# Optimization experiments

Hardware: AMD Instinct MI355X
Metric: run time of the kernel (lower is better)

The kernel has to match this reference:

```python
import jax, jax.numpy as jnp
import numpy as np

NUM_LEVELS = 4
RADIUS = 4


def _avg_pool2(x):
    # x: [N, H, W] -> 2x2 avg pool, stride 2, VALID (matches F.avg_pool2d(corr, 2, 2))
    s = jax.lax.reduce_window(x, 0.0, jax.lax.add, (1, 2, 2), (1, 2, 2), 'VALID')
    return s * 0.25


def _bilinear_sampler(img, coords):
    # img: [N, H, W]; coords: [N, K, K, 2] with (x, y) in pixel units.
    # Matches grid_sample(align_corners=True, padding_mode='zeros').
    N, H, W = img.shape
    x, y = coords[..., 0], coords[..., 1]
    x0 = jnp.floor(x)
    y0 = jnp.floor(y)
    nidx = jnp.arange(N)[:, None, None]

    def corner(xi, yi, w):
        valid = (xi >= 0) & (xi <= W - 1) & (yi >= 0) & (yi <= H - 1)
        xc = jnp.clip(xi, 0, W - 1).astype(jnp.int32)
        yc = jnp.clip(yi, 0, H - 1).astype(jnp.int32)
        return jnp.where(valid, img[nidx, yc, xc], 0.0) * w

    wx1 = x - x0
    wx0 = 1.0 - wx1
    wy1 = y - y0
    wy0 = 1.0 - wy1
    return (corner(x0, y0, wx0 * wy0) + corner(x0 + 1.0, y0, wx1 * wy0)
            + corner(x0, y0 + 1.0, wx0 * wy1) + corner(x0 + 1.0, y0 + 1.0, wx1 * wy1))


def setup_inputs() -> dict:
    key = jax.random.key(0)
    ks = jax.random.split(key, 8)
    B, C, H, W, D = 2, 256, 46, 96, 256
    fmap1 = jax.random.normal(ks[0], (B, C, H, W), jnp.float32)
    fmap2 = jax.random.normal(ks[1], (B, C, H, W), jnp.float32)
    ys, xs = jnp.meshgrid(jnp.arange(H, dtype=jnp.float32),
                          jnp.arange(W, dtype=jnp.float32), indexing='ij')
    base = jnp.broadcast_to(jnp.stack([xs, ys], 0), (B, 2, H, W))  # channels = (x, y)
    coords1 = base
    coords_lookup = base + 2.0 * jax.random.normal(ks[2], (B, 2, H, W), jnp.float32)
    Wf = jax.random.normal(ks[3], (C, D), jnp.float32) / np.sqrt(C).astype(np.float32)
    bf = jnp.zeros((D,), jnp.float32)
    Wpos = jax.random.normal(ks[4], (2, D), jnp.float32) * 0.003
    Wq = jax.random.normal(ks[5], (D, D), jnp.float32) / np.sqrt(D).astype(np.float32)
    Wk = jax.random.normal(ks[6], (D, D), jnp.float32) / np.sqrt(D).astype(np.float32)
    return {"fmap1": fmap1, "fmap2": fmap2, "coords1": coords1,
            "coords_lookup": coords_lookup, "Wf": Wf, "bf": bf,
            "Wpos": Wpos, "Wq": Wq, "Wk": Wk}


def reference(fmap1, fmap2, coords1, coords_lookup, Wf, bf, Wpos, Wq, Wk):
    B, C, H, W = fmap1.shape
    HW = H * W
    D = Wf.shape[1]
    dt = fmap1.dtype
    # --- update(): SETrans cross-attention correlation volume ---
    # coords2 = gen_all_indices -> full (y, x) grid
    ys, xs = jnp.meshgrid(jnp.arange(H, dtype=dt), jnp.arange(W, dtype=dt), indexing='ij')
    coords2_yx = jnp.broadcast_to(jnp.stack([ys, xs], -1), (B, H, W, 2)).reshape(B, HW, 2)
    # coords1 stored as (x, y) channels; permute(0,2,3,1).flip(-1) -> (y, x)
    coords1_yx = jnp.transpose(coords1, (0, 2, 3, 1))[..., ::-1].reshape(B, HW, 2)
    f1 = jnp.transpose(fmap1.reshape(B, C, HW), (0, 2, 1))  # [B, HW, C]
    f2 = jnp.transpose(fmap2.reshape(B, C, HW), (0, 2, 1))
    pos1 = coords1_yx @ Wpos                                  # [B, HW, D]
    pos2 = coords2_yx @ Wpos
    vispos1 = f1 @ Wf + bf + pos1
    vispos2 = f2 @ Wf + bf + pos2
    scale = jnp.sqrt(jnp.asarray(D, dt))
    pos_biases = jnp.einsum('bid,bjd->bij', pos1, pos2) / scale  # injected positional biases
    q = vispos1 @ Wq
    k = vispos2 @ Wk
    scores = jnp.einsum('bid,bjd->bij', q, k) / scale + pos_biases
    corr = jax.nn.softmax(scores, axis=-1)                    # [B, HW1, HW2] attn-prob correlation
    corr = corr.reshape(B * HW, H, W)
    pyramid = [corr]
    for _ in range(NUM_LEVELS - 1):
        corr = _avg_pool2(corr)
        pyramid.append(corr)
    # --- __call__(coords): multiscale bilinear lookup ---
    r = RADIUS
    d = jnp.linspace(-r, r, 2 * r + 1, dtype=dt)
    dyy, dxx = jnp.meshgrid(d, d, indexing='ij')              # matches torch.meshgrid(dy, dx)
    delta = jnp.stack([dyy, dxx], -1)[None]                   # [1, K, K, 2]
    cl = jnp.transpose(coords_lookup, (0, 2, 3, 1)).reshape(B * HW, 1, 1, 2)
    outs = []
    for i, lvl in enumerate(pyramid):
        coords_lvl = cl / (2.0 ** i) + delta                  # [B*HW, K, K, 2]
        samp = _bilinear_sampler(lvl, coords_lvl)             # [B*HW, K, K]
        outs.append(samp.reshape(B, H, W, -1))
    out = jnp.concatenate(outs, axis=-1)                      # [B, H, W, L*K*K]
    return jnp.transpose(out, (0, 3, 1, 2)).astype(jnp.float32)
```

## Files before the change

kernel.cpp:

```cpp
#include <hip/hip_runtime.h>
#include <cstdint>

typedef _Float16 f16;
typedef __attribute__((ext_vector_type(2))) _Float16 f16x2;
typedef __attribute__((ext_vector_type(4))) _Float16 f16x4;
typedef __attribute__((ext_vector_type(8))) _Float16 f16x8;
typedef __attribute__((ext_vector_type(4))) float f32x4;

#define NB 2
#define NH 46
#define NW 96
#define NHW 4416
#define ND 256
#define NTILES 276
#define SSTR 4424
#define L2E 1.44269504f

#define OFF_WFQ 0
#define OFF_WFK 131072
#define OFF_PQ  262144
#define OFF_PK  264192
#define OFF_BQ  266240
#define OFF_BK  267264
#define OFF_GS  268288
#define OFF_Q   268544
#define OFF_K   4790528
#define OFF_RM  9312512
#define OFF_S   9453824
#define SCOL    4432
#define WS_NEED 87740672UL

__global__ __launch_bounds__(256) void prep_kernel(
    const float* __restrict__ Wf, const float* __restrict__ bf,
    const float* __restrict__ Wpos, const float* __restrict__ Wq,
    const float* __restrict__ Wk, char* __restrict__ ws) {
  f16* WFQ = (f16*)(ws + OFF_WFQ);
  f16* WFK = (f16*)(ws + OFF_WFK);
  float* PQ = (float*)(ws + OFF_PQ);
  float* PK = (float*)(ws + OFF_PK);
  float* BQ = (float*)(ws + OFF_BQ);
  float* BK = (float*)(ws + OFF_BK);
  float* GS = (float*)(ws + OFF_GS);
  int bid = blockIdx.x, d = threadIdx.x;
  if (bid < 256) {
    int c = bid;
    float aq = 0.f, ak = 0.f;
#pragma unroll 8
    for (int t = 0; t < 256; ++t) {
      float wf = Wf[c * 256 + t];
      aq += wf * Wq[t * 256 + d];
      ak += wf * Wk[t * 256 + d];
    }
    WFQ[c * 256 + d] = (f16)(aq * 0.0625f);
    WFK[c * 256 + d] = (f16)ak;
  } else if (bid == 256) {
    float pq0 = 0, pq1 = 0, pk0 = 0, pk1 = 0, bq = 0, bk = 0;
#pragma unroll 4
    for (int c = 0; c < 256; ++c) {
      float wq = Wq[c * 256 + d], wk = Wk[c * 256 + d];
      pq0 += Wpos[c] * wq;       pq1 += Wpos[256 + c] * wq;
      pk0 += Wpos[c] * wk;       pk1 += Wpos[256 + c] * wk;
      bq  += bf[c] * wq;         bk  += bf[c] * wk;
    }
    PQ[d] = pq0 * 0.0625f; PQ[256 + d] = pq1 * 0.0625f;
    PK[d] = pk0;           PK[256 + d] = pk1;
    BQ[d] = bq * 0.0625f;  BK[d] = bk;
  } else if (d < 4) {
    int a = d >> 1, b2 = d & 1;
    float g = 0;
    for (int t = 0; t < 256; ++t) g += Wpos[a * 256 + t] * Wpos[b2 * 256 + t];
    GS[d] = g * 0.0625f;
  }
}

__global__ __launch_bounds__(256) void qk_gemm(
    const float* __restrict__ fmap1, const float* __restrict__ fmap2,
    const float* __restrict__ coords1, char* __restrict__ ws) {
  __shared__ f16 As[64 * 40];
  __shared__ f16 Bs[128 * 40];
  __shared__ float py[64], px[64];
  const int z = blockIdx.z;
  const float* fmap = z ? fmap2 : fmap1;
  const f16* Wt = (const f16*)(ws + (z ? OFF_WFK : OFF_WFQ));
  const float* P = (const float*)(ws + (z ? OFF_PK : OFF_PQ));
  const float* bias = (const float*)(ws + (z ? OFF_BK : OFF_BQ));
  f16* outb = (f16*)(ws + (z ? OFF_K : OFF_Q));
  const int t = threadIdx.x;
  const int g0 = blockIdx.x * 64;
  const int b = g0 / NHW;
  const int hwb = g0 - b * NHW;
  const int d0 = blockIdx.y * 128;
  if (t < 64) {
    int hw = hwb + t;
    if (z == 0) {
      py[t] = coords1[(b * 2 + 1) * NHW + hw];
      px[t] = coords1[(b * 2 + 0) * NHW + hw];
    } else {
      int y = hw / NW;
      py[t] = (float)y;
      px[t] = (float)(hw - y * NW);
    }
  }
  const int lane = t & 63, wave = t >> 6;
  const int wr = (wave >> 1) * 32, wc0 = (wave & 1) * 64;
  const int hwl = t & 63, cl0 = t >> 6;
  const int dd = t & 127, ch = t >> 7;
  f32x4 acc[2][4] = {};
  for (int kt = 0; kt < 8; ++kt) {
    int kk = kt * 32;
    __syncthreads();
#pragma unroll
    for (int i = 0; i < 8; ++i) {
      int c = cl0 + i * 4;
      As[hwl * 40 + c] = (f16)fmap[(size_t)(b * ND + kk + c) * NHW + hwb + hwl];
    }
#pragma unroll
    for (int i = 0; i < 16; ++i) {
      int c = ch * 16 + i;
      Bs[dd * 40 + c] = Wt[(kk + c) * ND + d0 + dd];
    }
    __syncthreads();
    int row = lane & 15, kq = (lane >> 4) * 8;
    f16x8 a0 = *(const f16x8*)&As[(wr + row) * 40 + kq];
    f16x8 a1 = *(const f16x8*)&As[(wr + 16 + row) * 40 + kq];
#pragma unroll
    for (int s = 0; s < 4; ++s) {
      f16x8 bs = *(const f16x8*)&Bs[(wc0 + 16 * s + row) * 40 + kq];
      acc[0][s] = __builtin_amdgcn_mfma_f32_16x16x32_f16(a0, bs, acc[0][s], 0, 0, 0);
      acc[1][s] = __builtin_amdgcn_mfma_f32_16x16x32_f16(a1, bs, acc[1][s], 0, 0, 0);
    }
  }
#pragma unroll
  for (int fi = 0; fi < 2; ++fi)
#pragma unroll
    for (int s = 0; s < 4; ++s)
#pragma unroll
      for (int r = 0; r < 4; ++r) {
        int rowl = wr + fi * 16 + (lane >> 4) * 4 + r;
        int d = d0 + wc0 + s * 16 + (lane & 15);
        float v = acc[fi][s][r] + bias[d] + py[rowl] * P[d] + px[rowl] * P[ND + d];
        outb[(size_t)(g0 + rowl) * ND + d] = (f16)v;
      }
}

__global__ __launch_bounds__(384, 2) void score_gemm(
    const float* __restrict__ coords1, char* __restrict__ ws) {
  __shared__ f16 kls[2][32][264];
  __shared__ f16 stw[6][16][36];
  __shared__ float u0s[96], u1s[96];
  const int tid = threadIdx.x;
  const int blk = blockIdx.x;
  const int xcd = blk & 7;
  const int b = xcd >> 2, nq = xcd & 3;
  const int hw0 = (blk >> 3) * 96;
  const int j00 = nq * 1104;
  const float* GS = (const float*)(ws + OFF_GS);
  if (tid < 96) {
    int hw = hw0 + tid;
    float cy = coords1[(b * 2 + 1) * NHW + hw];
    float cx = coords1[(b * 2 + 0) * NHW + hw];
    u0s[tid] = cy * GS[0] + cx * GS[2];
    u1s[tid] = cy * GS[1] + cx * GS[3];
  }
  const f16* __restrict__ qb = (const f16*)(ws + OFF_Q);
  const f16* __restrict__ kb = (const f16*)(ws + OFF_K);
  f16* __restrict__ gSb = (f16*)(ws + OFF_S) + ((size_t)b * NHW + hw0) * SCOL;
  float* __restrict__ rmG = (float*)(ws + OFF_RM);
  const int lane = tid & 63, wave = tid >> 6;
  const int q = lane & 15, h = lane >> 4;
  f16x8 qfrag[8];
#pragma unroll
  for (int ks = 0; ks < 8; ++ks)
    qfrag[ks] = *(const f16x8*)&qb[(size_t)(b * NHW + hw0 + wave * 16 + q) * ND + ks * 32 + h * 8];
  for (int c = tid; c < 32 * 32; c += 384) {
    int r = c >> 5, cc = c & 31;
    *(f16x8*)&kls[0][r][cc * 8] =
        *(const f16x8*)&kb[(size_t)(b * NHW + j00 + r) * ND + cc * 8];
  }
  __syncthreads();
  const float u0m = u0s[wave * 16 + q], u1m = u1s[wave * 16 + q];
  float pmax = -3e38f;
  const int srow = lane >> 2, scg = lane & 3;

  for (int it = 0; it <= 34; ++it) {
    const int buf = it & 1;
    const int jp = j00 + it * 32;
    const bool full = (it < 34);
    if (it < 34) {
      const int nW = (it < 33) ? 32 : 16;
      const int jn = j00 + (it + 1) * 32;
      for (int c = tid; c < nW * 32; c += 384) {
        int r = c >> 5, cc = c & 31;
        *(f16x8*)&kls[buf ^ 1][r][cc * 8] =
            *(const f16x8*)&kb[(size_t)(b * NHW + jn + r) * ND + cc * 8];
      }
    }
    f32x4 acc0 = {}, acc1 = {};
#pragma unroll
    for (int ks = 0; ks < 8; ++ks) {
      f16x8 kf = *(const f16x8*)&kls[buf][q][ks * 32 + h * 8];
      acc0 = __builtin_amdgcn_mfma_f32_16x16x32_f16(kf, qfrag[ks], acc0, 0, 0, 0);
    }
    if (full) {
#pragma unroll
      for (int ks = 0; ks < 8; ++ks) {
        f16x8 kf = *(const f16x8*)&kls[buf][16 + q][ks * 32 + h * 8];
        acc1 = __builtin_amdgcn_mfma_f32_16x16x32_f16(kf, qfrag[ks], acc1, 0, 0, 0);
      }
    }
    {
      f16x4 v0, v1;
#pragma unroll
      for (int r = 0; r < 4; ++r) {
        int j = jp + h * 4 + r;
        int yj = j / NW;
        float s = acc0[r] + u0m * (float)yj + u1m * (float)(j - yj * NW);
        pmax = fmaxf(pmax, s);
        v0[r] = (f16)s;
      }
      *(f16x4*)&stw[wave][q][h * 4] = v0;
      if (full) {
#pragma unroll
        for (int r = 0; r < 4; ++r) {
          int j = jp + 16 + h * 4 + r;
          int yj = j / NW;
          float s = acc1[r] + u0m * (float)yj + u1m * (float)(j - yj * NW);
          pmax = fmaxf(pmax, s);
          v1[r] = (f16)s;
        }
        *(f16x4*)&stw[wave][q][16 + h * 4] = v1;
      }
    }
    if (full) {
      f16x8 row8 = *(const f16x8*)&stw[wave][srow][scg * 8];
      *(f16x8*)&gSb[(size_t)(wave * 16 + srow) * SCOL + jp + scg * 8] = row8;
    } else {
      f16x4 row4 = *(const f16x4*)&stw[wave][srow][scg * 4];
      *(f16x4*)&gSb[(size_t)(wave * 16 + srow) * SCOL + jp + scg * 4] = row4;
    }
    __syncthreads();
  }
  pmax = fmaxf(pmax, __shfl_xor(pmax, 16));
  pmax = fmaxf(pmax, __shfl_xor(pmax, 32));
  if (lane < 16)
    rmG[((size_t)b * 4 + nq) * NHW + hw0 + wave * 16 + q] = pmax;
}

__global__ __launch_bounds__(512) void lookup_kernel(
    const float* __restrict__ clup, const char* __restrict__ ws,
    float* __restrict__ out) {
  __shared__ f16 lv1W[8][1104];
  __shared__ f16 lv2W[8][264];
  __shared__ f16 lv3W[8][60];
  __shared__ f16 winW[8][10][24];
  const int tid = threadIdx.x;
  const int blk0 = blockIdx.x;
  const int xcd = blk0 & 7;
  const int b = xcd >> 2;
  const int hw0 = ((blk0 >> 3) * 4 + (xcd & 3)) * 16;
  const f16* gS = (const f16*)(ws + OFF_S);
  const float* rmG = (const float*)(ws + OFF_RM);
  const int lane = tid & 63, wave = tid >> 6;
  f16* lv1 = lv1W[wave];
  f16* lv2 = lv2W[wave];
  f16* lv3 = lv3W[wave];

  for (int rr2 = 0; rr2 < 2; ++rr2) {
    const int r = wave * 2 + rr2;
    const int hw = hw0 + r;
    const size_t grow = (size_t)b * NHW + hw;
    const f16* sp = gS + grow * SCOL;
    const float clx = clup[(b * 2 + 0) * NHW + hw];
    const float cly = clup[(b * 2 + 1) * NHW + hw];
    const float* rp = rmG + (size_t)b * 4 * NHW + hw;
    const float m = fmaxf(fmaxf(rp[0], rp[NHW]), fmaxf(rp[2 * NHW], rp[3 * NHW]));
    const int wy0 = (int)floorf(cly) - 4;
    const int wx0 = (int)floorf(clx) - 4;
    const int xb = (wx0 >> 3) << 3;
    if (lane < 30) {
      int r10 = lane / 3, chk = lane - r10 * 3;
      int yy = wy0 + r10;
      int xc = xb + chk * 8;
      if (yy >= 0 && yy < NH) {
        if (xc >= 0 && xc + 8 <= NW) {
          *(f16x8*)&winW[wave][r10][chk * 8] = *(const f16x8*)&sp[yy * NW + xc];
        } else {
#pragma unroll
          for (int e = 0; e < 8; ++e) {
            int x = xc + e;
            winW[wave][r10][chk * 8 + e] =
                (x >= 0 && x < NW) ? sp[yy * NW + x] : (f16)0.f;
          }
        }
      }
    }
    float psum = 0.f;
    for (int u = lane; u < 276; u += 64) {
      int y1 = u / 12, g = u - y1 * 12;
      f16x8 A = *(const f16x8*)&sp[(2 * y1) * NW + g * 8];
      f16x8 B = *(const f16x8*)&sp[(2 * y1 + 1) * NW + g * 8];
      f16x4 v;
#pragma unroll
      for (int e = 0; e < 4; ++e) {
        float e00 = __builtin_amdgcn_exp2f(((float)A[2 * e] - m) * L2E);
        float e01 = __builtin_amdgcn_exp2f(((float)A[2 * e + 1] - m) * L2E);
        float e10 = __builtin_amdgcn_exp2f(((float)B[2 * e] - m) * L2E);
        float e11 = __builtin_amdgcn_exp2f(((float)B[2 * e + 1] - m) * L2E);
        float s4 = (e00 + e01) + (e10 + e11);
        v[e] = (f16)s4;
        psum += s4;
      }
      *(f16x4*)&lv1[y1 * 48 + g * 4] = v;
    }
#pragma unroll
    for (int off = 1; off < 64; off <<= 1) psum += __shfl_xor(psum, off);
    const float rinv = 1.f / psum;
    __threadfence_block();
    for (int c2 = lane; c2 < 264; c2 += 64) {
      int yy = c2 / 24, xx = c2 - yy * 24;
      f16x2 a = *(const f16x2*)&lv1[(2 * yy) * 48 + 2 * xx];
      f16x2 bb = *(const f16x2*)&lv1[(2 * yy + 1) * 48 + 2 * xx];
      lv2[c2] = (f16)(((float)a[0] + (float)a[1]) + ((float)bb[0] + (float)bb[1]));
    }
    __threadfence_block();
    if (lane < 60) {
      int yy = lane / 12, xx = lane - yy * 12;
      f16x2 a = *(const f16x2*)&lv2[(2 * yy) * 24 + 2 * xx];
      f16x2 bb = *(const f16x2*)&lv2[(2 * yy + 1) * 24 + 2 * xx];
      lv3[lane] = (f16)(((float)a[0] + (float)a[1]) + ((float)bb[0] + (float)bb[1]));
    }
    __threadfence_block();
    for (int c = lane; c < 324; c += 64) {
      int lvl = c / 81, rem = c - lvl * 81;
      int k0 = rem / 9, k1 = rem - k0 * 9;
      const float wdiv[4] = {1.f, 0.25f, 0.0625f, 0.015625f};
      const int Wi[4] = {96, 48, 24, 12}, Hi[4] = {46, 23, 11, 5};
      float xq = clx / (float)(1 << lvl) + (float)(k0 - 4);
      float yq = cly / (float)(1 << lvl) + (float)(k1 - 4);
      float x0f = floorf(xq), y0f = floorf(yq);
      int x0 = (int)x0f, y0 = (int)y0f;
      float wx1 = xq - x0f, wx0f_ = 1.f - wx1;
      float wy1 = yq - y0f, wy0f_ = 1.f - wy1;
      int Wl = Wi[lvl], Hl = Hi[lvl];
      float v = 0.f;
#pragma unroll
      for (int dy = 0; dy < 2; ++dy)
#pragma unroll
        for (int dx = 0; dx < 2; ++dx) {
          int xi = x0 + dx, yi = y0 + dy;
          if (xi >= 0 && xi < Wl && yi >= 0 && yi < Hl) {
            float pv;
            if (lvl == 0)
              pv = __builtin_amdgcn_exp2f(
                  ((float)winW[wave][yi - wy0][xi - xb] - m) * L2E);
            else if (lvl == 1) pv = (float)lv1[yi * 48 + xi];
            else if (lvl == 2) pv = (float)lv2[yi * 24 + xi];
            else               pv = (float)lv3[yi * 12 + xi];
            v += pv * (dx ? wx1 : wx0f_) * (dy ? wy1 : wy0f_);
          }
        }
      int hh = hw / NW, wcol = hw - hh * NW;
      int chn = lvl * 81 + k0 * 9 + k1;
      out[((size_t)(b * 324 + chn) * NH + hh) * NW + wcol] = v * wdiv[lvl] * rinv;
    }
    __threadfence_block();
  }
}

__global__ __launch_bounds__(1024) void attn_lookup(
    const float* __restrict__ coords1, const float* __restrict__ clup,
    const char* __restrict__ ws, float* __restrict__ out) {
  __shared__ f16 S[16 * SSTR];
  __shared__ f16 lv1[4][1104];
  __shared__ f16 lv2[4][264];
  __shared__ f16 lv3[4][60];
  __shared__ float wmax[16][16];
  __shared__ float wpart[16];
  __shared__ float u0s[16], u1s[16], clxs[16], clys[16], rinv[16], rowmaxS[16];
  const int tid = threadIdx.x;
  const int blk0 = blockIdx.x;
  const int xcd = blk0 & 7;
  const int b = xcd >> 2;
  const int hw0 = ((blk0 >> 3) * 4 + (xcd & 3)) * 16;
  const float* GS = (const float*)(ws + OFF_GS);
  if (tid < 16) {
    int hw = hw0 + tid;
    float cy = coords1[(b * 2 + 1) * NHW + hw];
    float cx = coords1[(b * 2 + 0) * NHW + hw];
    u0s[tid] = cy * GS[0] + cx * GS[2];
    u1s[tid] = cy * GS[1] + cx * GS[3];
    clxs[tid] = clup[(b * 2 + 0) * NHW + hw];
    clys[tid] = clup[(b * 2 + 1) * NHW + hw];
  }
  const f16* qb = (const f16*)(ws + OFF_Q);
  const f16* kb = (const f16*)(ws + OFF_K);
  const int lane = tid & 63;
  const int arow = lane & 15, akq = (lane >> 4) * 8;
  const int i0 = (lane >> 4) * 4;
  f16x8 afrag[8];
#pragma unroll
  for (int ks = 0; ks < 8; ++ks)
    afrag[ks] = *(const f16x8*)&qb[(size_t)(b * NHW + hw0 + arow) * ND + ks * 32 + akq];
  __syncthreads();
  float u0r[4], u1r[4];
#pragma unroll
  for (int r = 0; r < 4; ++r) { u0r[r] = u0s[i0 + r]; u1r[r] = u1s[i0 + r]; }
  const int wave = tid >> 6;
  float pmax[4] = {-3e38f, -3e38f, -3e38f, -3e38f};
  {
    const int cnt = (NTILES - wave + 15) / 16;
    const f16* kp = &kb[(size_t)(b * NHW + wave * 16 + arow) * ND + akq];
    const size_t tstep = (size_t)256 * ND;
    int nt = wave;
    f16x8 h0[4], h1[4];
#pragma unroll
    for (int s = 0; s < 4; ++s) h0[s] = *(const f16x8*)&kp[s * 32];
    for (int i = 0; i < cnt; ++i) {
      f32x4 acc0 = {}, acc1 = {};
#pragma unroll
      for (int s = 0; s < 4; ++s) h1[s] = *(const f16x8*)&kp[128 + s * 32];
      acc0 = __builtin_amdgcn_mfma_f32_16x16x32_f16(afrag[0], h0[0], acc0, 0, 0, 0);
      acc1 = __builtin_amdgcn_mfma_f32_16x16x32_f16(afrag[1], h0[1], acc1, 0, 0, 0);
      acc0 = __builtin_amdgcn_mfma_f32_16x16x32_f16(afrag[2], h0[2], acc0, 0, 0, 0);
      acc1 = __builtin_amdgcn_mfma_f32_16x16x32_f16(afrag[3], h0[3], acc1, 0, 0, 0);
      const f16* kpn = kp + tstep;
      if (i + 1 < cnt) {
#pragma unroll
        for (int s = 0; s < 4; ++s) h0[s] = *(const f16x8*)&kpn[s * 32];
      }
      acc0 = __builtin_amdgcn_mfma_f32_16x16x32_f16(afrag[4], h1[0], acc0, 0, 0, 0);
      acc1 = __builtin_amdgcn_mfma_f32_16x16x32_f16(afrag[5], h1[1], acc1, 0, 0, 0);
      acc0 = __builtin_amdgcn_mfma_f32_16x16x32_f16(afrag[6], h1[2], acc0, 0, 0, 0);
      acc1 = __builtin_amdgcn_mfma_f32_16x16x32_f16(afrag[7], h1[3], acc1, 0, 0, 0);
      int j = nt * 16 + (lane & 15);
      int yj = j / NW;
      float yf = (float)yj, xf = (float)(j - yj * NW);
#pragma unroll
      for (int r = 0; r < 4; ++r) {
        float s = acc0[r] + acc1[r] + u0r[r] * yf + u1r[r] * xf;
        pmax[r] = fmaxf(pmax[r], s);
        S[(i0 + r) * SSTR + j] = (f16)s;
      }
      kp = kpn; nt += 16;
    }
  }
#pragma unroll
  for (int off = 1; off < 16; off <<= 1)
#pragma unroll
    for (int r = 0; r < 4; ++r) pmax[r] = fmaxf(pmax[r], __shfl_xor(pmax[r], off));
  if ((lane & 15) == 0) {
#pragma unroll
    for (int r = 0; r < 4; ++r) wmax[wave][i0 + r] = pmax[r];
  }
  __syncthreads();
  if (tid < 16) {
    float m = wmax[0][tid];
#pragma unroll
    for (int w = 1; w < 16; ++w) m = fmaxf(m, wmax[w][tid]);
    rowmaxS[tid] = m;
  }
  __syncthreads();
  const int rgrp = tid >> 8, ts = tid & 255;
  for (int p = 0; p < 4; ++p) {
    const int r = p * 4 + rgrp;
    const f16* Sr = &S[r * SSTR];
    const float m = rowmaxS[r];
    float psum = 0.f;
    for (int c = ts; c < 1104; c += 256) {
      int yy = c / 48, xx = c - yy * 48;
      f16x2 a = *(const f16x2*)&Sr[(2 * yy) * NW + 2 * xx];
      f16x2 bb = *(const f16x2*)&Sr[(2 * yy + 1) * NW + 2 * xx];
      float e0 = __builtin_amdgcn_exp2f(((float)a[0] - m) * L2E);
      float e1 = __builtin_amdgcn_exp2f(((float)a[1] - m) * L2E);
      float e2 = __builtin_amdgcn_exp2f(((float)bb[0] - m) * L2E);
      float e3 = __builtin_amdgcn_exp2f(((float)bb[1] - m) * L2E);
      float s4 = (e0 + e1) + (e2 + e3);
      lv1[rgrp][c] = (f16)s4;
      psum += s4;
    }
#pragma unroll
    for (int off = 1; off < 64; off <<= 1) psum += __shfl_xor(psum, off);
    if (lane == 0) wpart[tid >> 6] = psum;
    __syncthreads();
    if (tid < 4)
      rinv[p * 4 + tid] = 1.f / (((wpart[tid * 4] + wpart[tid * 4 + 1]) +
                                  (wpart[tid * 4 + 2] + wpart[tid * 4 + 3])));
    for (int c2 = ts; c2 < 264; c2 += 256) {
      int yy = c2 / 24, xx = c2 - yy * 24;
      f16x2 a = *(const f16x2*)&lv1[rgrp][(2 * yy) * 48 + 2 * xx];
      f16x2 bb = *(const f16x2*)&lv1[rgrp][(2 * yy + 1) * 48 + 2 * xx];
      lv2[rgrp][c2] = (f16)(((float)a[0] + (float)a[1]) + ((float)bb[0] + (float)bb[1]));
    }
    __syncthreads();
    if (ts < 60) {
      int yy = ts / 12, xx = ts - yy * 12;
      f16x2 a = *(const f16x2*)&lv2[rgrp][(2 * yy) * 24 + 2 * xx];
      f16x2 bb = *(const f16x2*)&lv2[rgrp][(2 * yy + 1) * 24 + 2 * xx];
      lv3[rgrp][ts] = (f16)(((float)a[0] + (float)a[1]) + ((float)bb[0] + (float)bb[1]));
    }
    __syncthreads();
    for (int idx = tid; idx < 1296; idx += 1024) {
      int rl = idx / 324, c = idx - rl * 324;
      int rr = p * 4 + rl;
      int lvl = c / 81, rem = c - lvl * 81;
      int k0 = rem / 9, k1 = rem - k0 * 9;
      const float wdiv[4] = {1.f, 0.25f, 0.0625f, 0.015625f};
      const int Wi[4] = {96, 48, 24, 12}, Hi[4] = {46, 23, 11, 5};
      float m2 = rowmaxS[rr];
      float xq = clxs[rr] / (float)(1 << lvl) + (float)(k0 - 4);
      float yq = clys[rr] / (float)(1 << lvl) + (float)(k1 - 4);
      float x0f = floorf(xq), y0f = floorf(yq);
      int x0 = (int)x0f, y0 = (int)y0f;
      float wx1 = xq - x0f, wx0 = 1.f - wx1;
      float wy1 = yq - y0f, wy0 = 1.f - wy1;
      int Wl = Wi[lvl], Hl = Hi[lvl];
      float v = 0.f;
#pragma unroll
      for (int dy = 0; dy < 2; ++dy)
#pragma unroll
        for (int dx = 0; dx < 2; ++dx) {
          int xi = x0 + dx, yi = y0 + dy;
          if (xi >= 0 && xi < Wl && yi >= 0 && yi < Hl) {
            float pv;
            if (lvl == 0)
              pv = __builtin_amdgcn_exp2f(((float)S[rr * SSTR + yi * NW + xi] - m2) * L2E);
            else if (lvl == 1) pv = (float)lv1[rl][yi * 48 + xi];
            else if (lvl == 2) pv = (float)lv2[rl][yi * 24 + xi];
            else               pv = (float)lv3[rl][yi * 12 + xi];
            v += pv * (dx ? wx1 : wx0) * (dy ? wy1 : wy0);
          }
        }
      int hw = hw0 + rr;
      int h = hw / NW, w = hw - h * NW;
      int chn = lvl * 81 + k0 * 9 + k1;
      out[((size_t)(b * 324 + chn) * NH + h) * NW + w] = v * wdiv[lvl] * rinv[rr];
    }
    __syncthreads();
  }
}

extern "C" void kernel_launch(void* const* d_in, const int* in_sizes, int n_in,
                              void* d_out, int out_size, void* d_ws, size_t ws_size,
                              hipStream_t stream) {
  const float* fmap1 = (const float*)d_in[0];
  const float* fmap2 = (const float*)d_in[1];
  const float* coords1 = (const float*)d_in[2];
  const float* clup = (const float*)d_in[3];
  const float* Wf = (const float*)d_in[4];
  const float* bf = (const float*)d_in[5];
  const float* Wpos = (const float*)d_in[6];
  const float* Wq = (const float*)d_in[7];
  const float* Wk = (const float*)d_in[8];
  char* ws = (char*)d_ws;
  float* out = (float*)d_out;

  prep_kernel<<<dim3(258), dim3(256), 0, stream>>>(Wf, bf, Wpos, Wq, Wk, ws);
  qk_gemm<<<dim3(138, 2, 2), dim3(256), 0, stream>>>(fmap1, fmap2, coords1, ws);
  if (ws_size >= (size_t)WS_NEED) {
    score_gemm<<<dim3(46 * 8), dim3(384), 0, stream>>>(coords1, ws);
    lookup_kernel<<<dim3(NB * NTILES), dim3(512), 0, stream>>>(clup, ws, out);
  } else {
    attn_lookup<<<dim3(NB * NTILES), dim3(1024), 0, stream>>>(coords1, clup, ws, out);
  }
}
```

Before: 149.5 us.

## Widen per-block tiles in qk_gemm and score_gemm to reuse loaded operands

qk_gemm now computes all 256 output columns per block instead of splitting them across two y-blocks, so the fmap A-tile is loaded and converted once rather than twice. score_gemm gives each wave 32 query rows instead of 16, so every K tile staged in LDS feeds twice as many MFMAs, halving K traffic per query. The trade-off is fewer blocks (276 and 184 on a 256-CU part), more accumulator and qfrag registers, and occupancy hints reduced to 1 block for score_gemm, which risks lower latency hiding and idle CUs.

```diff
diff --git a/kernel.cpp b/kernel.cpp
--- a/kernel.cpp
+++ b/kernel.cpp
@@ -73,11 +73,11 @@
   }
 }
 
-__global__ __launch_bounds__(256) void qk_gemm(
+__global__ __launch_bounds__(256, 2) void qk_gemm(
     const float* __restrict__ fmap1, const float* __restrict__ fmap2,
     const float* __restrict__ coords1, char* __restrict__ ws) {
   __shared__ f16 As[64 * 40];
-  __shared__ f16 Bs[128 * 40];
+  __shared__ f16 Bs[256 * 40];
   __shared__ float py[64], px[64];
   const int z = blockIdx.z;
   const float* fmap = z ? fmap2 : fmap1;
@@ -89,7 +89,6 @@
   const int g0 = blockIdx.x * 64;
   const int b = g0 / NHW;
   const int hwb = g0 - b * NHW;
-  const int d0 = blockIdx.y * 128;
   if (t < 64) {
     int hw = hwb + t;
     if (z == 0) {
@@ -102,10 +101,10 @@
     }
   }
   const int lane = t & 63, wave = t >> 6;
-  const int wr = (wave >> 1) * 32, wc0 = (wave & 1) * 64;
+  const int wr = (wave >> 1) * 32, wc0 = (wave & 1) * 128;
   const int hwl = t & 63, cl0 = t >> 6;
   const int dd = t & 127, ch = t >> 7;
-  f32x4 acc[2][4] = {};
+  f32x4 acc[2][8] = {};
   for (int kt = 0; kt < 8; ++kt) {
     int kk = kt * 32;
     __syncthreads();
@@ -117,14 +116,15 @@
 #pragma unroll
     for (int i = 0; i < 16; ++i) {
       int c = ch * 16 + i;
-      Bs[dd * 40 + c] = Wt[(kk + c) * ND + d0 + dd];
+      Bs[dd * 40 + c] = Wt[(kk + c) * ND + dd];
+      Bs[(dd + 128) * 40 + c] = Wt[(kk + c) * ND + dd + 128];
     }
     __syncthreads();
     int row = lane & 15, kq = (lane >> 4) * 8;
     f16x8 a0 = *(const f16x8*)&As[(wr + row) * 40 + kq];
     f16x8 a1 = *(const f16x8*)&As[(wr + 16 + row) * 40 + kq];
 #pragma unroll
-    for (int s = 0; s < 4; ++s) {
+    for (int s = 0; s < 8; ++s) {
       f16x8 bs = *(const f16x8*)&Bs[(wc0 + 16 * s + row) * 40 + kq];
       acc[0][s] = __builtin_amdgcn_mfma_f32_16x16x32_f16(a0, bs, acc[0][s], 0, 0, 0);
       acc[1][s] = __builtin_amdgcn_mfma_f32_16x16x32_f16(a1, bs, acc[1][s], 0, 0, 0);
@@ -133,29 +133,29 @@
 #pragma unroll
   for (int fi = 0; fi < 2; ++fi)
 #pragma unroll
-    for (int s = 0; s < 4; ++s)
+    for (int s = 0; s < 8; ++s)
 #pragma unroll
       for (int r = 0; r < 4; ++r) {
         int rowl = wr + fi * 16 + (lane >> 4) * 4 + r;
-        int d = d0 + wc0 + s * 16 + (lane & 15);
+        int d = wc0 + s * 16 + (lane & 15);
         float v = acc[fi][s][r] + bias[d] + py[rowl] * P[d] + px[rowl] * P[ND + d];
         outb[(size_t)(g0 + rowl) * ND + d] = (f16)v;
       }
 }
 
-__global__ __launch_bounds__(384, 2) void score_gemm(
+__global__ __launch_bounds__(384, 1) void score_gemm(
     const float* __restrict__ coords1, char* __restrict__ ws) {
   __shared__ f16 kls[2][32][264];
-  __shared__ f16 stw[6][16][36];
-  __shared__ float u0s[96], u1s[96];
+  __shared__ f16 stw[6][32][36];
+  __shared__ float u0s[192], u1s[192];
   const int tid = threadIdx.x;
   const int blk = blockIdx.x;
   const int xcd = blk & 7;
   const int b = xcd >> 2, nq = xcd & 3;
-  const int hw0 = (blk >> 3) * 96;
+  const int hw0 = (blk >> 3) * 192;
   const int j00 = nq * 1104;
   const float* GS = (const float*)(ws + OFF_GS);
-  if (tid < 96) {
+  if (tid < 192) {
     int hw = hw0 + tid;
     float cy = coords1[(b * 2 + 1) * NHW + hw];
     float cx = coords1[(b * 2 + 0) * NHW + hw];
@@ -168,19 +168,23 @@
   float* __restrict__ rmG = (float*)(ws + OFF_RM);
   const int lane = tid & 63, wave = tid >> 6;
   const int q = lane & 15, h = lane >> 4;
-  f16x8 qfrag[8];
-#pragma unroll
-  for (int ks = 0; ks < 8; ++ks)
-    qfrag[ks] = *(const f16x8*)&qb[(size_t)(b * NHW + hw0 + wave * 16 + q) * ND + ks * 32 + h * 8];
+  const int wq0 = wave * 32;
+  f16x8 qfrag[2][8];
+#pragma unroll
+  for (int s = 0; s < 2; ++s)
+#pragma unroll
+    for (int ks = 0; ks < 8; ++ks)
+      qfrag[s][ks] = *(const f16x8*)&qb[(size_t)(b * NHW + hw0 + wq0 + s * 16 + q) * ND + ks * 32 + h * 8];
   for (int c = tid; c < 32 * 32; c += 384) {
     int r = c >> 5, cc = c & 31;
     *(f16x8*)&kls[0][r][cc * 8] =
         *(const f16x8*)&kb[(size_t)(b * NHW + j00 + r) * ND + cc * 8];
   }
   __syncthreads();
-  const float u0m = u0s[wave * 16 + q], u1m = u1s[wave * 16 + q];
-  float pmax = -3e38f;
-  const int srow = lane >> 2, scg = lane & 3;
+  const float u0a = u0s[wq0 + q], u1a = u1s[wq0 + q];
+  const float u0b = u0s[wq0 + 16 + q], u1b = u1s[wq0 + 16 + q];
+  float pmax0 = -3e38f, pmax1 = -3e38f;
+  const int srow = lane >> 1, scg = lane & 1;
 
   for (int it = 0; it <= 34; ++it) {
     const int buf = it & 1;
@@ -195,55 +199,80 @@
             *(const f16x8*)&kb[(size_t)(b * NHW + jn + r) * ND + cc * 8];
       }
     }
-    f32x4 acc0 = {}, acc1 = {};
+    f32x4 acc00 = {}, acc01 = {}, acc10 = {}, acc11 = {};
 #pragma unroll
     for (int ks = 0; ks < 8; ++ks) {
       f16x8 kf = *(const f16x8*)&kls[buf][q][ks * 32 + h * 8];
-      acc0 = __builtin_amdgcn_mfma_f32_16x16x32_f16(kf, qfrag[ks], acc0, 0, 0, 0);
+      acc00 = __builtin_amdgcn_mfma_f32_16x16x32_f16(kf, qfrag[0][ks], acc00, 0, 0, 0);
+      acc01 = __builtin_amdgcn_mfma_f32_16x16x32_f16(kf, qfrag[1][ks], acc01, 0, 0, 0);
     }
     if (full) {
 #pragma unroll
       for (int ks = 0; ks < 8; ++ks) {
         f16x8 kf = *(const f16x8*)&kls[buf][16 + q][ks * 32 + h * 8];
-        acc1 = __builtin_amdgcn_mfma_f32_16x16x32_f16(kf, qfrag[ks], acc1, 0, 0, 0);
+        acc10 = __builtin_amdgcn_mfma_f32_16x16x32_f16(kf, qfrag[0][ks], acc10, 0, 0, 0);
+        acc11 = __builtin_amdgcn_mfma_f32_16x16x32_f16(kf, qfrag[1][ks], acc11, 0, 0, 0);
       }
     }
     {
-      f16x4 v0, v1;
+      float yf0[4], xf0[4];
 #pragma unroll
       for (int r = 0; r < 4; ++r) {
         int j = jp + h * 4 + r;
         int yj = j / NW;
-        float s = acc0[r] + u0m * (float)yj + u1m * (float)(j - yj * NW);
-        pmax = fmaxf(pmax, s);
-        v0[r] = (f16)s;
-      }
-      *(f16x4*)&stw[wave][q][h * 4] = v0;
+        yf0[r] = (float)yj; xf0[r] = (float)(j - yj * NW);
+      }
+      f16x4 va, vb;
+#pragma unroll
+      for (int r = 0; r < 4; ++r) {
+        float s0 = acc00[r] + u0a * yf0[r] + u1a * xf0[r];
+        float s1 = acc01[r] + u0b * yf0[r] + u1b * xf0[r];
+        pmax0 = fmaxf(pmax0, s0);
+        pmax1 = fmaxf(pmax1, s1);
+        va[r] = (f16)s0; vb[r] = (f16)s1;
+      }
+      *(f16x4*)&stw[wave][q][h * 4] = va;
+      *(f16x4*)&stw[wave][16 + q][h * 4] = vb;
       if (full) {
+        float yf1[4], xf1[4];
 #pragma unroll
         for (int r = 0; r < 4; ++r) {
           int j = jp + 16 + h * 4 + r;
           int yj = j / NW;
-          float s = acc1[r] + u0m * (float)yj + u1m * (float)(j - yj * NW);
-          pmax = fmaxf(pmax, s);
-          v1[r] = (f16)s;
+          yf1[r] = (float)yj; xf1[r] = (float)(j - yj * NW);
         }
-        *(f16x4*)&stw[wave][q][16 + h * 4] = v1;
+#pragma unroll
+        for (int r = 0; r < 4; ++r) {
+          float s0 = acc10[r] + u0a * yf1[r] + u1a * xf1[r];
+          float s1 = acc11[r] + u0b * yf1[r] + u1b * xf1[r];
+          pmax0 = fmaxf(pmax0, s0);
+          pmax1 = fmaxf(pmax1, s1);
+          va[r] = (f16)s0; vb[r] = (f16)s1;
+        }
+        *(f16x4*)&stw[wave][q][16 + h * 4] = va;
+        *(f16x4*)&stw[wave][16 + q][16 + h * 4] = vb;
       }
     }
     if (full) {
-      f16x8 row8 = *(const f16x8*)&stw[wave][srow][scg * 8];
-      *(f16x8*)&gSb[(size_t)(wave * 16 + srow) * SCOL + jp + scg * 8] = row8;
+      f16x8 rA = *(const f16x8*)&stw[wave][srow][scg * 16];
+      f16x8 rB = *(const f16x8*)&stw[wave][srow][scg * 16 + 8];
+      f16* dst = &gSb[(size_t)(wq0 + srow) * SCOL + jp + scg * 16];
+      *(f16x8*)&dst[0] = rA;
+      *(f16x8*)&dst[8] = rB;
     } else {
-      f16x4 row4 = *(const f16x4*)&stw[wave][srow][scg * 4];
-      *(f16x4*)&gSb[(size_t)(wave * 16 + srow) * SCOL + jp + scg * 4] = row4;
-    }
-    __syncthreads();
-  }
-  pmax = fmaxf(pmax, __shfl_xor(pmax, 16));
-  pmax = fmaxf(pmax, __shfl_xor(pmax, 32));
-  if (lane < 16)
-    rmG[((size_t)b * 4 + nq) * NHW + hw0 + wave * 16 + q] = pmax;
+      f16x8 rA = *(const f16x8*)&stw[wave][srow][scg * 8];
+      *(f16x8*)&gSb[(size_t)(wq0 + srow) * SCOL + jp + scg * 8] = rA;
+    }
+    __syncthreads();
+  }
+  pmax0 = fmaxf(pmax0, __shfl_xor(pmax0, 16));
+  pmax0 = fmaxf(pmax0, __shfl_xor(pmax0, 32));
+  pmax1 = fmaxf(pmax1, __shfl_xor(pmax1, 16));
+  pmax1 = fmaxf(pmax1, __shfl_xor(pmax1, 32));
+  if (lane < 16) {
+    rmG[((size_t)b * 4 + nq) * NHW + hw0 + wq0 + q] = pmax0;
+    rmG[((size_t)b * 4 + nq) * NHW + hw0 + wq0 + 16 + q] = pmax1;
+  }
 }
 
 __global__ __launch_bounds__(512) void lookup_kernel(
@@ -555,9 +584,9 @@
   float* out = (float*)d_out;
 
   prep_kernel<<<dim3(258), dim3(256), 0, stream>>>(Wf, bf, Wpos, Wq, Wk, ws);
-  qk_gemm<<<dim3(138, 2, 2), dim3(256), 0, stream>>>(fmap1, fmap2, coords1, ws);
+  qk_gemm<<<dim3(138, 1, 2), dim3(256), 0, stream>>>(fmap1, fmap2, coords1, ws);
   if (ws_size >= (size_t)WS_NEED) {
-    score_gemm<<<dim3(46 * 8), dim3(384), 0, stream>>>(coords1, ws);
+    score_gemm<<<dim3(23 * 8), dim3(384), 0, stream>>>(coords1, ws);
     lookup_kernel<<<dim3(NB * NTILES), dim3(512), 0, stream>>>(clup, ws, out);
   } else {
     attn_lookup<<<dim3(NB * NTILES), dim3(1024), 0, stream>>>(coords1, clup, ws, out);
```

Result: faster. 145.6 us (-2.6%).
